# Kernel tuning notes

Measured on AMD Instinct MI355X. Metric: run time of the kernel, lower is better.

The kernel has to match this reference:

```python
import jax, jax.numpy as jnp
import numpy as np

N_SIN = 3  # fcn_n_sin

def _feats(x):
    # x: [B, Din] -> features [B, Din, 1 + 2*N_SIN]
    omega = (2.0 ** jnp.arange(N_SIN, dtype=x.dtype))  # [n_sin]
    ox = x[..., None] * omega  # [B, Din, n_sin]
    return jnp.concatenate([x[..., None], jnp.sin(ox), jnp.cos(ox)], axis=-1)

def setup_inputs() -> dict:
    key = jax.random.key(0)
    k1, k2, k3 = jax.random.split(key, 3)
    B, Din, Dout, H, F = 2048, 64, 64, 32, 1 + 2 * N_SIN
    x = jax.random.normal(k1, (B, Din), dtype=jnp.float32)
    # xavier-normal-ish init for W1/W2, zeros for biases (matches init_parameters)
    W1 = jax.random.normal(k2, (Din, Dout, H, F), dtype=jnp.float32) * np.sqrt(2.0 / (H + F))
    W2 = jax.random.normal(k3, (Din, Dout, 1, H), dtype=jnp.float32) * np.sqrt(2.0 / (1 + H))
    B1 = jnp.zeros((Din, Dout, H), dtype=jnp.float32)
    B2 = jnp.zeros((Din, Dout, 1), dtype=jnp.float32)
    return {"x": x, "W1": W1, "W2": W2, "B1": B1, "B2": B2}

def reference(x, W1, W2, B1, B2):
    f = _feats(x)  # [B, Din, F]
    # per-edge first layer: [B, Din, Dout, H]
    h = jnp.einsum('bif,iohf->bioh', f, W1) + B1[None]
    h = jax.nn.silu(h)
    # per-edge second layer -> scalar: [B, Din, Dout]
    phis = jnp.einsum('bioh,ioh->bio', h, W2[:, :, 0, :]) + B2[:, :, 0][None]
    return phis.sum(axis=1)  # [B, Dout]
```

## Files before the change

kernel.cpp:

```cpp
#include <hip/hip_runtime.h>
#include <math.h>

typedef _Float16 f16;
typedef f16   f16x4    __attribute__((ext_vector_type(4)));
typedef f16   f16x8    __attribute__((ext_vector_type(8)));
typedef float floatx4  __attribute__((ext_vector_type(4)));
typedef float floatx16 __attribute__((ext_vector_type(16)));

#define LOG2E 1.44269504088896340736f

#define B_SZ  2048
#define DIN   64
#define DOUT  64
#define NH    32

#define NIG   4
#define IGW   (DIN / NIG)

#define W1IMG_ELEMS ((size_t)DIN * DOUT * 64 * 4)
#define FIMG_ELEMS  ((size_t)DIN * 64 * 64 * 4)
#define W2Q_ELEMS   ((size_t)DIN * DOUT * NH)

__global__ __launch_bounds__(256) void prep_kernel(
        const float* __restrict__ W1, const float* __restrict__ B1,
        const float* __restrict__ W2, const float* __restrict__ B2,
        const float* __restrict__ x,
        f16* __restrict__ w1img, f16* __restrict__ fimg,
        float* __restrict__ w2q, float* __restrict__ b2sum,
        float* __restrict__ out) {
    const int bid = blockIdx.x, tid = threadIdx.x;
    if (bid < 512) {
        int u = bid * 256 + tid;
        int lane2 = u & 31, o = (u >> 5) & 63, i = u >> 11;
        int l0 = lane2 * 2;
        f16x8 v;
        if (lane2 < 16) {
#pragma unroll
            for (int t = 0; t < 2; ++t) {
                const float* w = W1 + (size_t)((i * 64 + o) * 32 + l0 + t) * 7;
#pragma unroll
                for (int j = 0; j < 4; ++j) v[t * 4 + j] = (f16)(w[j] * (-LOG2E));
            }
        } else {
#pragma unroll
            for (int t = 0; t < 2; ++t) {
                int m = l0 - 32 + t;
                const float* w = W1 + (size_t)((i * 64 + o) * 32 + m) * 7;
                v[t * 4 + 0] = (f16)(w[4] * (-LOG2E));
                v[t * 4 + 1] = (f16)(w[5] * (-LOG2E));
                v[t * 4 + 2] = (f16)(w[6] * (-LOG2E));
                v[t * 4 + 3] = (f16)(B1[(i * 64 + o) * 32 + m] * (-LOG2E));
            }
        }
        *(f16x8*)(w1img + (size_t)u * 8) = v;
    } else if (bid < 1024) {
        int u = (bid - 512) * 256 + tid;
        int lane2 = u & 31, btp = (u >> 5) & 63, i = u >> 11;
        int l0 = lane2 * 2;
        f16x8 v;
#pragma unroll
        for (int t = 0; t < 2; ++t) {
            int b = btp * 32 + ((l0 + t) & 31);
            float xv = x[b * 64 + i];
            float s1, c1;
            __sincosf(xv, &s1, &c1);
            float s2 = 2.0f * s1 * c1, c2 = 1.0f - 2.0f * s1 * s1;
            float s4 = 2.0f * s2 * c2, c4 = 1.0f - 2.0f * s2 * s2;
            if (lane2 < 16) { v[t*4+0] = (f16)xv; v[t*4+1] = (f16)s1;
                              v[t*4+2] = (f16)s2; v[t*4+3] = (f16)s4; }
            else            { v[t*4+0] = (f16)c1; v[t*4+1] = (f16)c2;
                              v[t*4+2] = (f16)c4; v[t*4+3] = (f16)1.0f; }
        }
        *(f16x8*)(fimg + (size_t)u * 8) = v;
    } else if (bid < 1152) {
        int t = (bid - 1024) * 256 + tid;
        floatx4 v = *(const floatx4*)(W2 + (size_t)t * 4);
        v *= (-1.0f / LOG2E);
        *(floatx4*)(w2q + (size_t)t * 4) = v;
    } else if (bid < 1280) {
        int t = (bid - 1152) * 256 + tid;
        floatx4 z = {};
        *(floatx4*)(out + (size_t)t * 4) = z;
    } else if (tid < 64) {
        float s = 0.0f;
        for (int i = 0; i < 64; ++i) s += B2[i * 64 + tid];
        b2sum[tid] = s;
    }
}

__global__ __launch_bounds__(128, 4) void main_kernel(
        const f16* __restrict__ w1img, const f16* __restrict__ fimg,
        const float* __restrict__ w2q, const float* __restrict__ b2sum,
        float* __restrict__ out) {
    const int tid  = threadIdx.x;
    const int lane = tid & 63;
    const int wv   = tid >> 6;
    const int btp  = blockIdx.x & 63;
    const int og   = (blockIdx.x >> 6) & 31;
    const int ig   = blockIdx.x >> 11;
    const int o    = __builtin_amdgcn_readfirstlane(og * 2 + wv);
    const int p    = lane >> 5;
    const size_t ibase = (size_t)ig * IGW;

    __shared__ float ws2[2][IGW][32];
    {
        int idx = tid * 8;
        int wv_ = idx >> 9, ii_ = (idx >> 5) & 15, h_ = idx & 31;
        const float* src = w2q + (ibase + ii_) * 2048
                         + (size_t)(og * 2 + wv_) * 32 + h_;
        *(floatx4*)&ws2[wv_][ii_][h_]     = *(const floatx4*)src;
        *(floatx4*)&ws2[wv_][ii_][h_ + 4] = *(const floatx4*)(src + 4);
    }
    __syncthreads();

    const f16* ap = w1img + ibase * 16384 + ((size_t)o   * 64 + lane) * 4;
    const f16* bp = fimg  + ibase * 16384 + ((size_t)btp * 64 + lane) * 4;

    f16x4 a = *(const f16x4*)ap;
    f16x4 b = *(const f16x4*)bp;

    float phi0 = 0.0f, phi1 = 0.0f, phi2 = 0.0f, phi3 = 0.0f;
    const floatx16 zeroC = {};

#pragma unroll 1
    for (int ii = 0; ii < IGW; ++ii) {
        const f16x4 ca = a, cb = b;

        const size_t i1 = (size_t)(ii + 1);
        a = *(const f16x4*)(ap + i1 * 16384);
        b = *(const f16x4*)(bp + i1 * 16384);

        const float* wrow = &ws2[wv][ii][p * 4];
        const floatx4 cw0 = *(const floatx4*)(wrow);
        const floatx4 cw1 = *(const floatx4*)(wrow + 8);
        const floatx4 cw2 = *(const floatx4*)(wrow + 16);
        const floatx4 cw3 = *(const floatx4*)(wrow + 24);

        floatx16 C = __builtin_amdgcn_mfma_f32_32x32x8f16(ca, cb, zeroC, 0, 0, 0);

#pragma unroll
        for (int r = 0; r < 4; ++r) {
            float av, e2, sg;
            av = C[0 + r];  e2 = __builtin_amdgcn_exp2f(av);
            sg = __builtin_amdgcn_rcpf(1.0f + e2);
            phi0 = __builtin_fmaf(av * cw0[r], sg, phi0);
            av = C[4 + r];  e2 = __builtin_amdgcn_exp2f(av);
            sg = __builtin_amdgcn_rcpf(1.0f + e2);
            phi1 = __builtin_fmaf(av * cw1[r], sg, phi1);
            av = C[8 + r];  e2 = __builtin_amdgcn_exp2f(av);
            sg = __builtin_amdgcn_rcpf(1.0f + e2);
            phi2 = __builtin_fmaf(av * cw2[r], sg, phi2);
            av = C[12 + r]; e2 = __builtin_amdgcn_exp2f(av);
            sg = __builtin_amdgcn_rcpf(1.0f + e2);
            phi3 = __builtin_fmaf(av * cw3[r], sg, phi3);
        }
    }

    float phi = (phi0 + phi1) + (phi2 + phi3);
    phi += __shfl_xor(phi, 32, 64);

    if (lane < 32) {
        float v = phi + 0.25f * b2sum[o];
        unsafeAtomicAdd(out + (size_t)(btp * 32 + lane) * 64 + o, v);
    }
}

extern "C" void kernel_launch(void* const* d_in, const int* in_sizes, int n_in,
                              void* d_out, int out_size, void* d_ws, size_t ws_size,
                              hipStream_t stream) {
    const float* x  = (const float*)d_in[0];
    const float* W1 = (const float*)d_in[1];
    const float* W2 = (const float*)d_in[2];
    const float* B1 = (const float*)d_in[3];
    const float* B2 = (const float*)d_in[4];
    float* out = (float*)d_out;

    f16*   w1img = (f16*)d_ws;
    f16*   fimg  = w1img + W1IMG_ELEMS;
    float* w2q   = (float*)(fimg + FIMG_ELEMS);
    float* b2sum = w2q + W2Q_ELEMS;

    prep_kernel<<<1281, 256, 0, stream>>>(W1, B1, W2, B2, x, w1img, fimg, w2q, b2sum, out);
    main_kernel<<<NIG * 32 * 64, 128, 0, stream>>>(w1img, fimg, w2q, b2sum, out);
}
```

Baseline: 128.6 us.

## Combine four sigmoid reciprocals into one rcp and deepen load prefetch

The per-element reciprocals of the sigmoid denominators are merged across four accumulator groups with a common-denominator fraction, so one rcp replaces four, at the cost of extra multiplies on float4 vectors. The global loads of the A and B fragments are prefetched two iterations ahead instead of one, and the shared W2 tile gets a padding row so the extra prefetch does not index past it. The product of four (1+exp2) terms can overflow float32 to inf when the pre-activations are strongly negative, which can give NaN or wrong values.

```diff
diff --git a/kernel.cpp b/kernel.cpp
--- a/kernel.cpp
+++ b/kernel.cpp
@@ -102,7 +102,7 @@
     const int p    = lane >> 5;
     const size_t ibase = (size_t)ig * IGW;
 
-    __shared__ float ws2[2][IGW][32];
+    __shared__ float ws2[2][IGW + 1][32];
     {
         int idx = tid * 8;
         int wv_ = idx >> 9, ii_ = (idx >> 5) & 15, h_ = idx & 31;
@@ -116,47 +116,59 @@
     const f16* ap = w1img + ibase * 16384 + ((size_t)o   * 64 + lane) * 4;
     const f16* bp = fimg  + ibase * 16384 + ((size_t)btp * 64 + lane) * 4;
 
-    f16x4 a = *(const f16x4*)ap;
-    f16x4 b = *(const f16x4*)bp;
+    f16x4 a0 = *(const f16x4*)ap;
+    f16x4 b0 = *(const f16x4*)bp;
+    f16x4 a1 = *(const f16x4*)(ap + 16384);
+    f16x4 b1 = *(const f16x4*)(bp + 16384);
 
-    float phi0 = 0.0f, phi1 = 0.0f, phi2 = 0.0f, phi3 = 0.0f;
+    floatx4 phiv = {};
     const floatx16 zeroC = {};
 
 #pragma unroll 1
     for (int ii = 0; ii < IGW; ++ii) {
-        const f16x4 ca = a, cb = b;
-
-        const size_t i1 = (size_t)(ii + 1);
-        a = *(const f16x4*)(ap + i1 * 16384);
-        b = *(const f16x4*)(bp + i1 * 16384);
+        const f16x4 ca = a0, cb = b0;
+        a0 = a1; b0 = b1;
+        const size_t i2 = (size_t)(ii + 2);
+        a1 = *(const f16x4*)(ap + i2 * 16384);
+        b1 = *(const f16x4*)(bp + i2 * 16384);
 
         const float* wrow = &ws2[wv][ii][p * 4];
-        const floatx4 cw0 = *(const floatx4*)(wrow);
-        const floatx4 cw1 = *(const floatx4*)(wrow + 8);
-        const floatx4 cw2 = *(const floatx4*)(wrow + 16);
-        const floatx4 cw3 = *(const floatx4*)(wrow + 24);
+        const floatx4 CW0 = *(const floatx4*)(wrow);
+        const floatx4 CW1 = *(const floatx4*)(wrow + 8);
+        const floatx4 CW2 = *(const floatx4*)(wrow + 16);
+        const floatx4 CW3 = *(const floatx4*)(wrow + 24);
 
         floatx16 C = __builtin_amdgcn_mfma_f32_32x32x8f16(ca, cb, zeroC, 0, 0, 0);
 
+        floatx4 A0 = {C[0],  C[1],  C[2],  C[3]};
+        floatx4 A1v = {C[4],  C[5],  C[6],  C[7]};
+        floatx4 A2 = {C[8],  C[9],  C[10], C[11]};
+        floatx4 A3 = {C[12], C[13], C[14], C[15]};
+
+        floatx4 E0, E1, E2, E3;
 #pragma unroll
-        for (int r = 0; r < 4; ++r) {
-            float av, e2, sg;
-            av = C[0 + r];  e2 = __builtin_amdgcn_exp2f(av);
-            sg = __builtin_amdgcn_rcpf(1.0f + e2);
-            phi0 = __builtin_fmaf(av * cw0[r], sg, phi0);
-            av = C[4 + r];  e2 = __builtin_amdgcn_exp2f(av);
-            sg = __builtin_amdgcn_rcpf(1.0f + e2);
-            phi1 = __builtin_fmaf(av * cw1[r], sg, phi1);
-            av = C[8 + r];  e2 = __builtin_amdgcn_exp2f(av);
-            sg = __builtin_amdgcn_rcpf(1.0f + e2);
-            phi2 = __builtin_fmaf(av * cw2[r], sg, phi2);
-            av = C[12 + r]; e2 = __builtin_amdgcn_exp2f(av);
-            sg = __builtin_amdgcn_rcpf(1.0f + e2);
-            phi3 = __builtin_fmaf(av * cw3[r], sg, phi3);
+        for (int j = 0; j < 4; ++j) {
+            E0[j] = __builtin_amdgcn_exp2f(A0[j]);
+            E1[j] = __builtin_amdgcn_exp2f(A1v[j]);
+            E2[j] = __builtin_amdgcn_exp2f(A2[j]);
+            E3[j] = __builtin_amdgcn_exp2f(A3[j]);
         }
+        floatx4 D0 = E0 + 1.0f, D1 = E1 + 1.0f;
+        floatx4 D2 = E2 + 1.0f, D3 = E3 + 1.0f;
+        floatx4 U0 = A0 * CW0, U1 = A1v * CW1;
+        floatx4 U2 = A2 * CW2, U3 = A3 * CW3;
+        floatx4 N01 = U0 * D1 + U1 * D0;
+        floatx4 N23 = U2 * D3 + U3 * D2;
+        floatx4 P01 = D0 * D1, P23 = D2 * D3;
+        floatx4 N   = N01 * P23 + N23 * P01;
+        floatx4 DD  = P01 * P23;
+        floatx4 R;
+#pragma unroll
+        for (int j = 0; j < 4; ++j) R[j] = __builtin_amdgcn_rcpf(DD[j]);
+        phiv = phiv + N * R;
     }
 
-    float phi = (phi0 + phi1) + (phi2 + phi3);
+    float phi = (phiv[0] + phiv[1]) + (phiv[2] + phiv[3]);
     phi += __shfl_xor(phi, 32, 64);
 
     if (lane < 32) {
```

New measurement: 112.8 us. 1.14x faster.

## Batch sigmoid reciprocals with packed FP32 math and software-pipeline the MFMA

Applied to the files above, without the earlier changes.

The per-element SiLU epilogue used one reciprocal per activation. It now combines four sigmoid terms over a common denominator, so a group of eight activations needs two reciprocals, and the adds and multiplies use packed v_pk_* FP32 instructions. The MFMA for the next input feature is issued one iteration ahead, global loads are prefetched two iterations ahead, and the occupancy hint rises from 4 to 6 waves per SIMD. Multiplying four (1+e) terms together can overflow or lose precision for large activations. The loop also reads one row past the input group, which is why the shared-memory weight array gains an extra row, and the added live registers may cost occupancy. The prep kernel's sincos call is replaced by the hardware sin/cos builtins on a pre-scaled argument.

```diff
diff --git a/kernel.cpp b/kernel.cpp
--- a/kernel.cpp
+++ b/kernel.cpp
@@ -4,10 +4,12 @@
 typedef _Float16 f16;
 typedef f16   f16x4    __attribute__((ext_vector_type(4)));
 typedef f16   f16x8    __attribute__((ext_vector_type(8)));
+typedef float floatx2  __attribute__((ext_vector_type(2)));
 typedef float floatx4  __attribute__((ext_vector_type(4)));
 typedef float floatx16 __attribute__((ext_vector_type(16)));
 
-#define LOG2E 1.44269504088896340736f
+#define LOG2E   1.44269504088896340736f
+#define INV_2PI 0.15915494309189533577f
 
 #define B_SZ  2048
 #define DIN   64
@@ -20,6 +22,16 @@
 #define W1IMG_ELEMS ((size_t)DIN * DOUT * 64 * 4)
 #define FIMG_ELEMS  ((size_t)DIN * 64 * 64 * 4)
 #define W2Q_ELEMS   ((size_t)DIN * DOUT * NH)
+
+__device__ __forceinline__ floatx2 pk_add(floatx2 a, floatx2 b) {
+    floatx2 d; asm("v_pk_add_f32 %0, %1, %2" : "=v"(d) : "v"(a), "v"(b)); return d;
+}
+__device__ __forceinline__ floatx2 pk_mul(floatx2 a, floatx2 b) {
+    floatx2 d; asm("v_pk_mul_f32 %0, %1, %2" : "=v"(d) : "v"(a), "v"(b)); return d;
+}
+__device__ __forceinline__ floatx2 pk_fma(floatx2 a, floatx2 b, floatx2 c) {
+    floatx2 d; asm("v_pk_fma_f32 %0, %1, %2, %3" : "=v"(d) : "v"(a), "v"(b), "v"(c)); return d;
+}
 
 __global__ __launch_bounds__(256) void prep_kernel(
         const float* __restrict__ W1, const float* __restrict__ B1,
@@ -62,8 +74,8 @@
         for (int t = 0; t < 2; ++t) {
             int b = btp * 32 + ((l0 + t) & 31);
             float xv = x[b * 64 + i];
-            float s1, c1;
-            __sincosf(xv, &s1, &c1);
+            float s1 = __builtin_amdgcn_sinf(xv * INV_2PI);
+            float c1 = __builtin_amdgcn_cosf(xv * INV_2PI);
             float s2 = 2.0f * s1 * c1, c2 = 1.0f - 2.0f * s1 * s1;
             float s4 = 2.0f * s2 * c2, c4 = 1.0f - 2.0f * s2 * s2;
             if (lane2 < 16) { v[t*4+0] = (f16)xv; v[t*4+1] = (f16)s1;
@@ -88,7 +100,28 @@
     }
 }
 
-__global__ __launch_bounds__(128, 4) void main_kernel(
+__device__ __forceinline__ void silu8(
+        floatx2 A0, floatx2 A1, floatx2 A2, floatx2 A3,
+        floatx2 W0, floatx2 W1, floatx2 W2, floatx2 W3,
+        floatx2 one2, floatx2& phi) {
+    floatx2 E0 = {__builtin_amdgcn_exp2f(A0[0]), __builtin_amdgcn_exp2f(A0[1])};
+    floatx2 E1 = {__builtin_amdgcn_exp2f(A1[0]), __builtin_amdgcn_exp2f(A1[1])};
+    floatx2 E2 = {__builtin_amdgcn_exp2f(A2[0]), __builtin_amdgcn_exp2f(A2[1])};
+    floatx2 E3 = {__builtin_amdgcn_exp2f(A3[0]), __builtin_amdgcn_exp2f(A3[1])};
+    floatx2 D0 = pk_add(E0, one2), D1 = pk_add(E1, one2);
+    floatx2 D2 = pk_add(E2, one2), D3 = pk_add(E3, one2);
+    floatx2 U0 = pk_mul(A0, W0), U1 = pk_mul(A1, W1);
+    floatx2 U2 = pk_mul(A2, W2), U3 = pk_mul(A3, W3);
+    floatx2 N01 = pk_fma(U0, D1, pk_mul(U1, D0));
+    floatx2 N23 = pk_fma(U2, D3, pk_mul(U3, D2));
+    floatx2 P01 = pk_mul(D0, D1), P23 = pk_mul(D2, D3);
+    floatx2 N   = pk_fma(N01, P23, pk_mul(N23, P01));
+    floatx2 DD  = pk_mul(P01, P23);
+    floatx2 R = {__builtin_amdgcn_rcpf(DD[0]), __builtin_amdgcn_rcpf(DD[1])};
+    phi = pk_fma(N, R, phi);
+}
+
+__global__ __launch_bounds__(128, 6) void main_kernel(
         const f16* __restrict__ w1img, const f16* __restrict__ fimg,
         const float* __restrict__ w2q, const float* __restrict__ b2sum,
         float* __restrict__ out) {
@@ -102,7 +135,7 @@
     const int p    = lane >> 5;
     const size_t ibase = (size_t)ig * IGW;
 
-    __shared__ float ws2[2][IGW][32];
+    __shared__ float ws2[2][IGW + 1][32];
     {
         int idx = tid * 8;
         int wv_ = idx >> 9, ii_ = (idx >> 5) & 15, h_ = idx & 31;
@@ -116,47 +149,44 @@
     const f16* ap = w1img + ibase * 16384 + ((size_t)o   * 64 + lane) * 4;
     const f16* bp = fimg  + ibase * 16384 + ((size_t)btp * 64 + lane) * 4;
 
-    f16x4 a = *(const f16x4*)ap;
-    f16x4 b = *(const f16x4*)bp;
-
-    float phi0 = 0.0f, phi1 = 0.0f, phi2 = 0.0f, phi3 = 0.0f;
     const floatx16 zeroC = {};
+    const floatx2  one2  = {1.0f, 1.0f};
+    floatx2 phiL = {}, phiH = {};
+
+    f16x4 a0v = *(const f16x4*)ap;
+    f16x4 b0v = *(const f16x4*)bp;
+    f16x4 a_n = *(const f16x4*)(ap + 16384);
+    f16x4 b_n = *(const f16x4*)(bp + 16384);
+    floatx16 Ccur = __builtin_amdgcn_mfma_f32_32x32x8f16(a0v, b0v, zeroC, 0, 0, 0);
 
 #pragma unroll 1
     for (int ii = 0; ii < IGW; ++ii) {
-        const f16x4 ca = a, cb = b;
-
-        const size_t i1 = (size_t)(ii + 1);
-        a = *(const f16x4*)(ap + i1 * 16384);
-        b = *(const f16x4*)(bp + i1 * 16384);
+        floatx16 Cn = __builtin_amdgcn_mfma_f32_32x32x8f16(a_n, b_n, zeroC, 0, 0, 0);
+        const size_t i2 = (size_t)(ii + 2);
+        a_n = *(const f16x4*)(ap + i2 * 16384);
+        b_n = *(const f16x4*)(bp + i2 * 16384);
 
         const float* wrow = &ws2[wv][ii][p * 4];
-        const floatx4 cw0 = *(const floatx4*)(wrow);
-        const floatx4 cw1 = *(const floatx4*)(wrow + 8);
-        const floatx4 cw2 = *(const floatx4*)(wrow + 16);
-        const floatx4 cw3 = *(const floatx4*)(wrow + 24);
-
-        floatx16 C = __builtin_amdgcn_mfma_f32_32x32x8f16(ca, cb, zeroC, 0, 0, 0);
-
-#pragma unroll
-        for (int r = 0; r < 4; ++r) {
-            float av, e2, sg;
-            av = C[0 + r];  e2 = __builtin_amdgcn_exp2f(av);
-            sg = __builtin_amdgcn_rcpf(1.0f + e2);
-            phi0 = __builtin_fmaf(av * cw0[r], sg, phi0);
-            av = C[4 + r];  e2 = __builtin_amdgcn_exp2f(av);
-            sg = __builtin_amdgcn_rcpf(1.0f + e2);
-            phi1 = __builtin_fmaf(av * cw1[r], sg, phi1);
-            av = C[8 + r];  e2 = __builtin_amdgcn_exp2f(av);
-            sg = __builtin_amdgcn_rcpf(1.0f + e2);
-            phi2 = __builtin_fmaf(av * cw2[r], sg, phi2);
-            av = C[12 + r]; e2 = __builtin_amdgcn_exp2f(av);
-            sg = __builtin_amdgcn_rcpf(1.0f + e2);
-            phi3 = __builtin_fmaf(av * cw3[r], sg, phi3);
-        }
-    }
-
-    float phi = (phi0 + phi1) + (phi2 + phi3);
+        const floatx4 W0 = *(const floatx4*)(wrow);
+        const floatx4 W1v = *(const floatx4*)(wrow + 8);
+        const floatx4 W2v = *(const floatx4*)(wrow + 16);
+        const floatx4 W3v = *(const floatx4*)(wrow + 24);
+
+        silu8((floatx2){Ccur[0],  Ccur[1]},  (floatx2){Ccur[4],  Ccur[5]},
+              (floatx2){Ccur[8],  Ccur[9]},  (floatx2){Ccur[12], Ccur[13]},
+              (floatx2){W0[0], W0[1]}, (floatx2){W1v[0], W1v[1]},
+              (floatx2){W2v[0], W2v[1]}, (floatx2){W3v[0], W3v[1]},
+              one2, phiL);
+        silu8((floatx2){Ccur[2],  Ccur[3]},  (floatx2){Ccur[6],  Ccur[7]},
+              (floatx2){Ccur[10], Ccur[11]}, (floatx2){Ccur[14], Ccur[15]},
+              (floatx2){W0[2], W0[3]}, (floatx2){W1v[2], W1v[3]},
+              (floatx2){W2v[2], W2v[3]}, (floatx2){W3v[2], W3v[3]},
+              one2, phiH);
+
+        Ccur = Cn;
+    }
+
+    float phi = (phiL[0] + phiL[1]) + (phiH[0] + phiH[1]);
     phi += __shfl_xor(phi, 32, 64);
 
     if (lane < 32) {
```

Measured after the change: 114.1 us. 1.13x faster.
